# Kernel tuning notes

Measured on AMD Instinct MI355X. Metric: run time of the kernel, lower is better.

The kernel has to match this reference:

```python
import jax, jax.numpy as jnp
import numpy as np

EMB = 768
N_HEADS = 12
HEAD_DIM = EMB // N_HEADS


def setup_inputs() -> dict:
    key = jax.random.key(0)
    k_x, k_w1, k_b1, k_w2, k_b2 = jax.random.split(key, 5)
    B, T = 8, 1024
    s = 0.02
    return {
        "x": jax.random.normal(k_x, (B, T, EMB), dtype=jnp.float32),
        "w_attn": jax.random.normal(k_w1, (EMB, 3 * EMB), dtype=jnp.float32) * s,
        "b_attn": jax.random.normal(k_b1, (3 * EMB,), dtype=jnp.float32) * s,
        "w_proj": jax.random.normal(k_w2, (EMB, EMB), dtype=jnp.float32) * s,
        "b_proj": jax.random.normal(k_b2, (EMB,), dtype=jnp.float32) * s,
    }


def reference(x, w_attn, b_attn, w_proj, b_proj):
    B, T, C = x.shape
    qkv = x @ w_attn + b_attn                       # [B,T,3C]
    q, k, v = jnp.split(qkv, 3, axis=2)
    # [B,T,C] -> [B,H,T,D]
    q = q.reshape(B, T, N_HEADS, HEAD_DIM).transpose(0, 2, 1, 3)
    k = k.reshape(B, T, N_HEADS, HEAD_DIM).transpose(0, 2, 1, 3)
    v = v.reshape(B, T, N_HEADS, HEAD_DIM).transpose(0, 2, 1, 3)
    scale = HEAD_DIM ** -0.5
    att = jnp.einsum("bhqd,bhkd->bhqk", q, k) * scale  # [B,H,T,T]
    causal = jnp.tril(jnp.ones((T, T), dtype=bool))
    att = jnp.where(causal, att, -jnp.inf)
    att = jax.nn.softmax(att, axis=-1)
    out = jnp.einsum("bhqk,bhkd->bhqd", att, v)        # [B,H,T,D]
    out = out.transpose(0, 2, 1, 3).reshape(B, T, C)
    return out @ w_proj + b_proj
```

## Files before the change

### kernel.cpp

```cpp
#include <hip/hip_runtime.h>
#include <hip/hip_bf16.h>
#include <math.h>

#define BATCH 8
#define SEQ   1024
#define EMB   768
#define NH    12
#define HD    64
#define QKVW  (3 * EMB)
#define VOFF  (2 * EMB)

typedef short short8   __attribute__((ext_vector_type(8)));
typedef float floatx4  __attribute__((ext_vector_type(4)));

__device__ __forceinline__ short f2bf(float f) {
    union { float f; unsigned u; } v; v.f = f;
    unsigned r = (v.u + 0x7fffu + ((v.u >> 16) & 1u)) >> 16;
    return (short)r;
}

__device__ __forceinline__ void async_load16(const void* g, void* l) {
    __builtin_amdgcn_global_load_lds(
        (const __attribute__((address_space(1))) unsigned int*)g,
        (__attribute__((address_space(3))) unsigned int*)l, 16, 0, 0);
}

#define CVT_NB 3072
#define TA_NB  1728
#define PREP_NB (CVT_NB + TA_NB + 576)

__global__ __launch_bounds__(256) void prep(
    const float* __restrict__ x, const float* __restrict__ w_attn,
    const float* __restrict__ w_proj, short* __restrict__ xb,
    short* __restrict__ waT, short* __restrict__ wpT)
{
    __shared__ float t[32][33];
    const int bid = blockIdx.x;
    const int tid = threadIdx.x;

    if (bid < CVT_NB) {
        const int i = bid * 256 + tid;
        const float4 a = ((const float4*)x)[2 * i];
        const float4 b = ((const float4*)x)[2 * i + 1];
        short8 s;
        s[0] = f2bf(a.x); s[1] = f2bf(a.y); s[2] = f2bf(a.z); s[3] = f2bf(a.w);
        s[4] = f2bf(b.x); s[5] = f2bf(b.y); s[6] = f2bf(b.z); s[7] = f2bf(b.w);
        ((short8*)xb)[i] = s;
        return;
    }

    const float* in; short* outT; int ncb, idx;
    if (bid < CVT_NB + TA_NB) { idx = bid - CVT_NB; in = w_attn; outT = waT; ncb = QKVW / 32; }
    else                      { idx = bid - CVT_NB - TA_NB; in = w_proj; outT = wpT; ncb = EMB / 32; }
    const int C  = ncb * 32;
    const int c0 = (idx % ncb) * 32;
    const int r0 = (idx / ncb) * 32;
    const int lx = tid & 31, ly = tid >> 5;
    #pragma unroll
    for (int i = 0; i < 32; i += 8)
        t[ly + i][lx] = in[(size_t)(r0 + ly + i) * C + c0 + lx];
    __syncthreads();
    #pragma unroll
    for (int i = 0; i < 32; i += 8)
        outT[(size_t)(c0 + ly + i) * EMB + r0 + lx] = f2bf(t[lx][ly + i]);
}

#define NT12 (EMB / 64)

#define BAR()    do { asm volatile("" ::: "memory"); __builtin_amdgcn_s_barrier(); \
                      asm volatile("" ::: "memory"); } while (0)
#define LGKM0()  asm volatile("s_waitcnt lgkmcnt(0)" ::: "memory")
#define VMC0()   asm volatile("s_waitcnt vmcnt(0)" ::: "memory")
#define VMC4()   asm volatile("s_waitcnt vmcnt(4)" ::: "memory")
#define SCHED0() __builtin_amdgcn_sched_barrier(0)
#define PRIO1()  __builtin_amdgcn_s_setprio(1)
#define PRIO0()  __builtin_amdgcn_s_setprio(0)

#define LDA(bf_, r_, q_) (*(const short8*)&As[bf_][(r_) * 64 + ((((q_)) ^ ((r_) & 7)) << 3)])
#define LDB(bf_, r_, q_) (*(const short8*)&Bs[bf_][(r_) * 64 + ((((q_)) ^ ((r_) & 7)) << 3)])

#define MMA_T(JB, NJ)                                                        \
    _Pragma("unroll")                                                        \
    for (int kk = 0; kk < 2; ++kk)                                           \
        _Pragma("unroll")                                                    \
        for (int mi = 0; mi < 4; ++mi)                                       \
            _Pragma("unroll")                                                \
            for (int nj = 0; nj < (NJ); ++nj)                                \
                acc[mi][(JB) + nj] =                                         \
                    __builtin_amdgcn_mfma_f32_16x16x32_bf16(                 \
                        b[(JB) + nj][kk], a[mi][kk],                         \
                        acc[mi][(JB) + nj], 0, 0, 0);

#define MMA_D(JB, NJ)                                                        \
    _Pragma("unroll")                                                        \
    for (int kk = 0; kk < 2; ++kk)                                           \
        _Pragma("unroll")                                                    \
        for (int mi = 0; mi < 4; ++mi)                                       \
            _Pragma("unroll")                                                \
            for (int nj = 0; nj < (NJ); ++nj)                                \
                acc[mi][(JB) + nj] =                                         \
                    __builtin_amdgcn_mfma_f32_16x16x32_bf16(                 \
                        a[mi][kk], b[(JB) + nj][kk],                         \
                        acc[mi][(JB) + nj], 0, 0, 0);

#define QCW   96
#define QNBX  (QKVW / QCW)
#define PNBX  (EMB / QCW)

#define KLOOPQ(MM)                                                           \
    for (int kt = 0; kt < NT12; ++kt) {                                      \
        const int buf = kt & 1;                                              \
            \
        _Pragma("unroll")                                                    \
        for (int mi = 0; mi < 4; ++mi)                                       \
            _Pragma("unroll")                                                \
            for (int kk = 0; kk < 2; ++kk)                                   \
                a[mi][kk] = LDA(buf, ar0 + mi * 16, quad + kk * 4);          \
        _Pragma("unroll")                                                    \
        for (int nj = 0; nj < 2; ++nj)                                       \
            _Pragma("unroll")                                                \
            for (int kk = 0; kk < 2; ++kk)                                   \
                b[nj][kk] = LDB(buf, br0 + nj * 16, quad + kk * 4);          \
        if (kt + 1 < NT12) stage_B(kt + 1);                                  \
        BAR(); LGKM0(); SCHED0();                                            \
        PRIO1(); MM(0, 2); PRIO0();                                          \
        BAR();                                                               \
                \
        _Pragma("unroll")                                                    \
        for (int kk = 0; kk < 2; ++kk)                                       \
            b[2][kk] = LDB(buf, br0 + 2 * 16, quad + kk * 4);                \
        if (kt + 2 < NT12) stage_A(kt + 2);                                  \
        BAR(); LGKM0(); SCHED0();                                            \
        PRIO1(); MM(2, 1); PRIO0();                                          \
        if (kt + 2 < NT12) { VMC4(); } else if (kt + 1 < NT12) { VMC0(); }   \
        BAR();                                                               \
    }

template <int MODE>
__global__ __launch_bounds__(256, 2) void gemm96(
    const short* __restrict__ A, const short* __restrict__ Bt,
    const float* __restrict__ bias, void* __restrict__ Cout,
    short* __restrict__ vt, int nbx)
{
    __shared__ __align__(16) short As[2][128 * 64];
    __shared__ __align__(16) short Bs[2][ 96 * 64];

    const int tid  = threadIdx.x;
    const int wave = tid >> 6;
    const int lane = tid & 63;
    const int ln15 = lane & 15;
    const int quad = lane >> 4;
    const int wm   = wave >> 1;
    const int wn   = wave & 1;

    const int orig = blockIdx.x;
    const int wg   = (orig & 7) * (8 * nbx) + (orig >> 3);
    const int bx   = wg % nbx;
    const int by   = wg / nbx;
    const int row0 = by * 128;
    const int col0 = bx * QCW;
    const bool vpath = (MODE == 1) && (col0 >= VOFF);

    const short* Ag = A  + (size_t)row0 * EMB;
    const short* Bg = Bt + (size_t)col0 * EMB;

    auto stage_A = [&](int t) {
        const int buf = t & 1;
        #pragma unroll
        for (int p = 0; p < 4; ++p) {
            const int id  = p * 256 + tid;
            const int row = id >> 3;
            const int c   = (id & 7) ^ (row & 7);
            async_load16(Ag + (size_t)row * EMB + t * 64 + c * 8, &As[buf][id * 8]);
        }
    };
    auto stage_B = [&](int t) {
        const int buf = t & 1;
        #pragma unroll
        for (int p = 0; p < 3; ++p) {
            const int id  = p * 256 + tid;
            const int row = id >> 3;
            const int c   = (id & 7) ^ (row & 7);
            async_load16(Bg + (size_t)row * EMB + t * 64 + c * 8, &Bs[buf][id * 8]);
        }
    };

    floatx4 acc[4][3];
    #pragma unroll
    for (int i = 0; i < 4; ++i)
        #pragma unroll
        for (int j = 0; j < 3; ++j) acc[i][j] = (floatx4){0.f, 0.f, 0.f, 0.f};

    short8 a[4][2];
    short8 b[3][2];

    stage_A(0); stage_B(0); stage_A(1);
    VMC4();
    BAR();

    const int ar0 = wm * 64 + ln15;
    const int br0 = wn * 48 + ln15;

    if (vpath) { KLOOPQ(MMA_D) } else { KLOOPQ(MMA_T) }

    const int wr = wm * 64, wc = wn * 48;
    if (MODE == 0) {
        float* Cf = (float*)Cout;
        float4 b4[3];
        #pragma unroll
        for (int j = 0; j < 3; ++j)
            b4[j] = *(const float4*)&bias[col0 + wc + j * 16 + quad * 4];
        #pragma unroll
        for (int i = 0; i < 4; ++i) {
            const int r = row0 + wr + i * 16 + ln15;
            #pragma unroll
            for (int j = 0; j < 3; ++j) {
                const int c = col0 + wc + j * 16 + quad * 4;
                float4 v;
                v.x = acc[i][j][0] + b4[j].x;
                v.y = acc[i][j][1] + b4[j].y;
                v.z = acc[i][j][2] + b4[j].z;
                v.w = acc[i][j][3] + b4[j].w;
                *(float4*)&Cf[(size_t)r * EMB + c] = v;
            }
        }
    } else if (!vpath) {
        short* Cs = (short*)Cout;
        #pragma unroll
        for (int j = 0; j < 3; ++j) {
            const float4 b4 = *(const float4*)&bias[col0 + wc + j * 16 + quad * 4];
            #pragma unroll
            for (int i = 0; i < 4; ++i) {
                const int r = row0 + wr + i * 16 + ln15;
                const int c = col0 + wc + j * 16 + quad * 4;
                union { short s[4]; unsigned long long u; } pk;
                pk.s[0] = f2bf(acc[i][j][0] + b4.x);
                pk.s[1] = f2bf(acc[i][j][1] + b4.y);
                pk.s[2] = f2bf(acc[i][j][2] + b4.z);
                pk.s[3] = f2bf(acc[i][j][3] + b4.w);
                *(unsigned long long*)&Cs[(size_t)r * QKVW + c] = pk.u;
            }
        }
    } else {
        #pragma unroll
        for (int j = 0; j < 3; ++j) {
            const int c  = col0 + wc + j * 16 + ln15;
            const float bv = bias[c];
            const int c2 = c - VOFF;
            #pragma unroll
            for (int i = 0; i < 4; ++i) {
                const int r = row0 + wr + i * 16 + quad * 4;
                union { short s[4]; unsigned long long u; } pk;
                #pragma unroll
                for (int reg = 0; reg < 4; ++reg)
                    pk.s[reg] = f2bf(acc[i][j][reg] + bv);
                *(unsigned long long*)&vt[(size_t)(r >> 10) * (EMB * SEQ) +
                                          (size_t)c2 * SEQ + (r & 1023)] = pk.u;
            }
        }
    }
}

#define LDK 72

__global__ __launch_bounds__(512) void attn_mfma(
    const short* __restrict__ qkv, const short* __restrict__ vt,
    short* __restrict__ out)
{
    __shared__ __align__(16) short Ks[2][64 * LDK];
    __shared__ __align__(16) short Vt[2][64 * LDK];
    __shared__ __align__(16) short Ps[8 * 16 * LDK];

    const int tid  = threadIdx.x;
    const int wave = tid >> 6;
    const int lane = tid & 63;
    const int ln15 = lane & 15;
    const int quad = lane >> 4;

    const int qc = 7 - (int)(blockIdx.x / (BATCH * NH));
    const int bh = blockIdx.x % (BATCH * NH);
    const int h  = bh % NH;
    const int b  = bh / NH;

    const int q0w = qc * 128 + wave * 16;

    const short* qkv_b = qkv + (size_t)b * SEQ * QKVW + h * HD;
    const short* Kg  = qkv_b + EMB;
    const short* Vtg = vt + ((size_t)b * EMB + h * HD) * SEQ;

    short8 qf[2];
    {
        const short* qrow = qkv_b + (size_t)(q0w + ln15) * QKVW;
        qf[0] = *(const short8*)(qrow + quad * 8);
        qf[1] = *(const short8*)(qrow + quad * 8 + 32);
    }

    floatx4 o[4];
    #pragma unroll
    for (int i = 0; i < 4; ++i) o[i] = (floatx4){0.f, 0.f, 0.f, 0.f};
    float lp[4] = {0.f, 0.f, 0.f, 0.f};

    const int rr = tid >> 3;
    const int c8 = (tid & 7) * 8;

    const int nkt = 2 * qc + 2;

    uint4 kreg = *(const uint4*)(Kg  + (size_t)rr * QKVW + c8);
    uint4 vreg = *(const uint4*)(Vtg + (size_t)rr * SEQ + c8);
    *(uint4*)&Ks[0][rr * LDK + c8] = kreg;
    *(uint4*)&Vt[0][rr * LDK + c8] = vreg;
    kreg = *(const uint4*)(Kg  + (size_t)(64 + rr) * QKVW + c8);
    vreg = *(const uint4*)(Vtg + (size_t)rr * SEQ + 64 + c8);

    for (int kt = 0; kt < nkt; ++kt) {
        const int cb = kt & 1;
        __syncthreads();

        floatx4 s[4];
        #pragma unroll
        for (int i = 0; i < 4; ++i) s[i] = (floatx4){0.f, 0.f, 0.f, 0.f};
        #pragma unroll
        for (int st = 0; st < 2; ++st)
            #pragma unroll
            for (int sub = 0; sub < 4; ++sub) {
                const short8 kf = *(const short8*)&Ks[cb][(ln15 + sub * 16) * LDK + quad * 8 + st * 32];
                s[sub] = __builtin_amdgcn_mfma_f32_16x16x32_bf16(qf[st], kf, s[sub], 0, 0, 0);
            }

        #pragma unroll
        for (int sub = 0; sub < 4; ++sub)
            #pragma unroll
            for (int reg = 0; reg < 4; ++reg) {
                float pv = __expf(s[sub][reg] * 0.125f);
                if (kt * 64 + ln15 + sub * 16 > q0w + quad * 4 + reg) pv = 0.f;
                s[sub][reg] = pv;
            }
        #pragma unroll
        for (int reg = 0; reg < 4; ++reg)
            lp[reg] += (s[0][reg] + s[1][reg]) + (s[2][reg] + s[3][reg]);

        short* Pw = &Ps[wave * 16 * LDK];
        #pragma unroll
        for (int sub = 0; sub < 4; ++sub)
            #pragma unroll
            for (int reg = 0; reg < 4; ++reg) {
                const int qr   = quad * 4 + reg;
                const int kr8  = sub * 2 + (ln15 >> 3);
                const int slot = (kr8 + 5 * quad + reg) & 7;
                Pw[qr * LDK + slot * 8 + (ln15 & 7)] = f2bf(s[sub][reg]);
            }

        short8 pf[2];
        #pragma unroll
        for (int st = 0; st < 2; ++st) {
            const int slot = ((quad + 4 * st) + 5 * (ln15 >> 2) + (ln15 & 3)) & 7;
            pf[st] = *(const short8*)&Pw[ln15 * LDK + slot * 8];
        }

        #pragma unroll
        for (int st = 0; st < 2; ++st)
            #pragma unroll
            for (int sub = 0; sub < 4; ++sub) {
                const short8 vf = *(const short8*)&Vt[cb][(ln15 + sub * 16) * LDK + quad * 8 + st * 32];
                o[sub] = __builtin_amdgcn_mfma_f32_16x16x32_bf16(pf[st], vf, o[sub], 0, 0, 0);
            }

        if (kt + 1 < nkt) {
            *(uint4*)&Ks[cb ^ 1][rr * LDK + c8] = kreg;
            *(uint4*)&Vt[cb ^ 1][rr * LDK + c8] = vreg;
            if (kt + 2 < nkt) {
                kreg = *(const uint4*)(Kg  + (size_t)((kt + 2) * 64 + rr) * QKVW + c8);
                vreg = *(const uint4*)(Vtg + (size_t)rr * SEQ + (kt + 2) * 64 + c8);
            }
        }
    }

    #pragma unroll
    for (int reg = 0; reg < 4; ++reg) {
        float t = lp[reg];
        #pragma unroll
        for (int off = 1; off <= 8; off <<= 1)
            t += __shfl_xor(t, off, 64);
        const float inv = 1.0f / t;
        const size_t row = (size_t)(b * SEQ + q0w + quad * 4 + reg) * EMB + h * HD;
        #pragma unroll
        for (int sub = 0; sub < 4; ++sub)
            out[row + ln15 + sub * 16] = f2bf(o[sub][reg] * inv);
    }
}

extern "C" void kernel_launch(void* const* d_in, const int* in_sizes, int n_in,
                              void* d_out, int out_size, void* d_ws, size_t ws_size,
                              hipStream_t stream)
{
    const float* x      = (const float*)d_in[0];
    const float* w_attn = (const float*)d_in[1];
    const float* b_attn = (const float*)d_in[2];
    const float* w_proj = (const float*)d_in[3];
    const float* b_proj = (const float*)d_in[4];
    float* out = (float*)d_out;

    const int M = BATCH * SEQ;

    short* xb    = (short*)d_ws;
    short* waT   = xb    + (size_t)M * EMB;
    short* wpT   = waT   + (size_t)QKVW * EMB;
    short* qkvb  = wpT   + (size_t)EMB * EMB;
    short* vtb   = qkvb  + (size_t)M * QKVW;
    short* attnb = vtb   + (size_t)BATCH * EMB * SEQ;

    prep<<<dim3(PREP_NB), dim3(256), 0, stream>>>(x, w_attn, w_proj, xb, waT, wpT);

    gemm96<1><<<dim3((M / 128) * QNBX), dim3(256), 0, stream>>>(
        xb, waT, b_attn, qkvb, vtb, QNBX);

    attn_mfma<<<dim3(8 * BATCH * NH), dim3(512), 0, stream>>>(qkvb, vtb, attnb);

    gemm96<0><<<dim3((M / 128) * PNBX), dim3(256), 0, stream>>>(
        attnb, wpT, b_proj, out, nullptr, PNBX);
}
```

Before: 183.1 us.

## Widen projection GEMM tiles to 128x192 with six waves per block

Both the QKV and output projection GEMMs now use a 128x192 output tile computed by 6 waves (2x3), up from 128x96 with 4 waves. Each wave covers a 64x64 sub-tile with a 4x4 accumulator. Only the first four waves load A, while all six load B, so wait counts differ per wave. This gives more reuse of each loaded A tile and fewer blocks, at the cost of more LDS and registers per block, lower block-count parallelism, and a 3-per-CU occupancy hint.

Result: slower. 194.6 us (+6.3%).

```diff
diff --git a/kernel.cpp b/kernel.cpp
--- a/kernel.cpp
+++ b/kernel.cpp
@@ -76,99 +76,101 @@
 #define PRIO1()  __builtin_amdgcn_s_setprio(1)
 #define PRIO0()  __builtin_amdgcn_s_setprio(0)
 
-#define LDA(bf_, r_, q_) (*(const short8*)&As[bf_][(r_) * 64 + ((((q_)) ^ ((r_) & 7)) << 3)])
-#define LDB(bf_, r_, q_) (*(const short8*)&Bs[bf_][(r_) * 64 + ((((q_)) ^ ((r_) & 7)) << 3)])
-
-#define MMA_T(JB, NJ)                                                        \
+#define LDA8(bf_, r_, q_) (*(const short8*)&As[bf_][(r_) * 64 + ((((q_)) ^ ((r_) & 7)) << 3)])
+#define LDB8(bf_, r_, q_) (*(const short8*)&Bs[bf_][(r_) * 64 + ((((q_)) ^ ((r_) & 7)) << 3)])
+
+#define MMA_T2(JB)                                                           \
     _Pragma("unroll")                                                        \
     for (int kk = 0; kk < 2; ++kk)                                           \
         _Pragma("unroll")                                                    \
         for (int mi = 0; mi < 4; ++mi)                                       \
             _Pragma("unroll")                                                \
-            for (int nj = 0; nj < (NJ); ++nj)                                \
+            for (int nj = 0; nj < 2; ++nj)                                   \
                 acc[mi][(JB) + nj] =                                         \
                     __builtin_amdgcn_mfma_f32_16x16x32_bf16(                 \
                         b[(JB) + nj][kk], a[mi][kk],                         \
                         acc[mi][(JB) + nj], 0, 0, 0);
 
-#define MMA_D(JB, NJ)                                                        \
+#define MMA_D2(JB)                                                           \
     _Pragma("unroll")                                                        \
     for (int kk = 0; kk < 2; ++kk)                                           \
         _Pragma("unroll")                                                    \
         for (int mi = 0; mi < 4; ++mi)                                       \
             _Pragma("unroll")                                                \
-            for (int nj = 0; nj < (NJ); ++nj)                                \
+            for (int nj = 0; nj < 2; ++nj)                                   \
                 acc[mi][(JB) + nj] =                                         \
                     __builtin_amdgcn_mfma_f32_16x16x32_bf16(                 \
                         a[mi][kk], b[(JB) + nj][kk],                         \
                         acc[mi][(JB) + nj], 0, 0, 0);
 
-#define QCW   96
-#define QNBX  (QKVW / QCW)
-#define PNBX  (EMB / QCW)
-
-#define KLOOPQ(MM)                                                           \
+#define KLOOP2(MM)                                                           \
     for (int kt = 0; kt < NT12; ++kt) {                                      \
         const int buf = kt & 1;                                              \
-            \
+                 \
         _Pragma("unroll")                                                    \
         for (int mi = 0; mi < 4; ++mi)                                       \
             _Pragma("unroll")                                                \
             for (int kk = 0; kk < 2; ++kk)                                   \
-                a[mi][kk] = LDA(buf, ar0 + mi * 16, quad + kk * 4);          \
+                a[mi][kk] = LDA8(buf, ar0 + mi * 16, quad + kk * 4);         \
         _Pragma("unroll")                                                    \
         for (int nj = 0; nj < 2; ++nj)                                       \
             _Pragma("unroll")                                                \
             for (int kk = 0; kk < 2; ++kk)                                   \
-                b[nj][kk] = LDB(buf, br0 + nj * 16, quad + kk * 4);          \
+                b[nj][kk] = LDB8(buf, br0 + nj * 16, quad + kk * 4);         \
         if (kt + 1 < NT12) stage_B(kt + 1);                                  \
         BAR(); LGKM0(); SCHED0();                                            \
-        PRIO1(); MM(0, 2); PRIO0();                                          \
+        PRIO1(); MM(0); PRIO0();                                             \
         BAR();                                                               \
-                \
+                     \
         _Pragma("unroll")                                                    \
-        for (int kk = 0; kk < 2; ++kk)                                       \
-            b[2][kk] = LDB(buf, br0 + 2 * 16, quad + kk * 4);                \
+        for (int nj = 2; nj < 4; ++nj)                                       \
+            _Pragma("unroll")                                                \
+            for (int kk = 0; kk < 2; ++kk)                                   \
+                b[nj][kk] = LDB8(buf, br0 + nj * 16, quad + kk * 4);         \
         if (kt + 2 < NT12) stage_A(kt + 2);                                  \
         BAR(); LGKM0(); SCHED0();                                            \
-        PRIO1(); MM(2, 1); PRIO0();                                          \
-        if (kt + 2 < NT12) { VMC4(); } else if (kt + 1 < NT12) { VMC0(); }   \
+        PRIO1(); MM(2); PRIO0();                                             \
+        if (kt + 2 < NT12) {                                                 \
+            if (wuni < 4) { VMC4(); } else { VMC0(); }                       \
+        } else if (kt + 1 < NT12) { VMC0(); }                                \
         BAR();                                                               \
     }
 
 template <int MODE>
-__global__ __launch_bounds__(256, 2) void gemm96(
+__global__ __launch_bounds__(384, 3) void gemm192(
     const short* __restrict__ A, const short* __restrict__ Bt,
     const float* __restrict__ bias, void* __restrict__ Cout,
     short* __restrict__ vt, int nbx)
 {
     __shared__ __align__(16) short As[2][128 * 64];
-    __shared__ __align__(16) short Bs[2][ 96 * 64];
+    __shared__ __align__(16) short Bs[2][192 * 64];
 
     const int tid  = threadIdx.x;
     const int wave = tid >> 6;
     const int lane = tid & 63;
     const int ln15 = lane & 15;
     const int quad = lane >> 4;
-    const int wm   = wave >> 1;
-    const int wn   = wave & 1;
+    const int wm   = wave / 3;
+    const int wn   = wave % 3;
+    const int wuni = __builtin_amdgcn_readfirstlane(wave);
 
     const int orig = blockIdx.x;
     const int wg   = (orig & 7) * (8 * nbx) + (orig >> 3);
     const int bx   = wg % nbx;
     const int by   = wg / nbx;
     const int row0 = by * 128;
-    const int col0 = bx * QCW;
+    const int col0 = bx * 192;
     const bool vpath = (MODE == 1) && (col0 >= VOFF);
 
     const short* Ag = A  + (size_t)row0 * EMB;
     const short* Bg = Bt + (size_t)col0 * EMB;
 
     auto stage_A = [&](int t) {
+        if (wave >= 4) return;
         const int buf = t & 1;
         #pragma unroll
         for (int p = 0; p < 4; ++p) {
-            const int id  = p * 256 + tid;
+            const int id  = (wave * 4 + p) * 64 + lane;
             const int row = id >> 3;
             const int c   = (id & 7) ^ (row & 7);
             async_load16(Ag + (size_t)row * EMB + t * 64 + c * 8, &As[buf][id * 8]);
@@ -177,44 +179,44 @@
     auto stage_B = [&](int t) {
         const int buf = t & 1;
         #pragma unroll
-        for (int p = 0; p < 3; ++p) {
-            const int id  = p * 256 + tid;
+        for (int p = 0; p < 4; ++p) {
+            const int id  = (wave * 4 + p) * 64 + lane;
             const int row = id >> 3;
             const int c   = (id & 7) ^ (row & 7);
             async_load16(Bg + (size_t)row * EMB + t * 64 + c * 8, &Bs[buf][id * 8]);
         }
     };
 
-    floatx4 acc[4][3];
+    floatx4 acc[4][4];
     #pragma unroll
     for (int i = 0; i < 4; ++i)
         #pragma unroll
-        for (int j = 0; j < 3; ++j) acc[i][j] = (floatx4){0.f, 0.f, 0.f, 0.f};
+        for (int j = 0; j < 4; ++j) acc[i][j] = (floatx4){0.f, 0.f, 0.f, 0.f};
 
     short8 a[4][2];
-    short8 b[3][2];
+    short8 b[4][2];
 
     stage_A(0); stage_B(0); stage_A(1);
-    VMC4();
+    if (wuni < 4) { VMC4(); } else { VMC0(); }
     BAR();
 
     const int ar0 = wm * 64 + ln15;
-    const int br0 = wn * 48 + ln15;
-
-    if (vpath) { KLOOPQ(MMA_D) } else { KLOOPQ(MMA_T) }
-
-    const int wr = wm * 64, wc = wn * 48;
+    const int br0 = wn * 64 + ln15;
+
+    if (vpath) { KLOOP2(MMA_D2) } else { KLOOP2(MMA_T2) }
+
+    const int wr = wm * 64, wc = wn * 64;
     if (MODE == 0) {
         float* Cf = (float*)Cout;
-        float4 b4[3];
-        #pragma unroll
-        for (int j = 0; j < 3; ++j)
+        float4 b4[4];
+        #pragma unroll
+        for (int j = 0; j < 4; ++j)
             b4[j] = *(const float4*)&bias[col0 + wc + j * 16 + quad * 4];
         #pragma unroll
         for (int i = 0; i < 4; ++i) {
             const int r = row0 + wr + i * 16 + ln15;
             #pragma unroll
-            for (int j = 0; j < 3; ++j) {
+            for (int j = 0; j < 4; ++j) {
                 const int c = col0 + wc + j * 16 + quad * 4;
                 float4 v;
                 v.x = acc[i][j][0] + b4[j].x;
@@ -227,7 +229,7 @@
     } else if (!vpath) {
         short* Cs = (short*)Cout;
         #pragma unroll
-        for (int j = 0; j < 3; ++j) {
+        for (int j = 0; j < 4; ++j) {
             const float4 b4 = *(const float4*)&bias[col0 + wc + j * 16 + quad * 4];
             #pragma unroll
             for (int i = 0; i < 4; ++i) {
@@ -243,7 +245,7 @@
         }
     } else {
         #pragma unroll
-        for (int j = 0; j < 3; ++j) {
+        for (int j = 0; j < 4; ++j) {
             const int c  = col0 + wc + j * 16 + ln15;
             const float bv = bias[c];
             const int c2 = c - VOFF;
@@ -411,11 +413,11 @@
 
     prep<<<dim3(PREP_NB), dim3(256), 0, stream>>>(x, w_attn, w_proj, xb, waT, wpT);
 
-    gemm96<1><<<dim3((M / 128) * QNBX), dim3(256), 0, stream>>>(
-        xb, waT, b_attn, qkvb, vtb, QNBX);
+    gemm192<1><<<dim3((M / 128) * (QKVW / 192)), dim3(384), 0, stream>>>(
+        xb, waT, b_attn, qkvb, vtb, QKVW / 192);
 
     attn_mfma<<<dim3(8 * BATCH * NH), dim3(512), 0, stream>>>(qkvb, vtb, attnb);
 
-    gemm96<0><<<dim3((M / 128) * PNBX), dim3(256), 0, stream>>>(
-        attnb, wpT, b_proj, out, nullptr, PNBX);
-}
+    gemm192<0><<<dim3((M / 128) * (EMB / 192)), dim3(384), 0, stream>>>(
+        attnb, wpT, b_proj, out, nullptr, EMB / 192);
+}
```
